# Optimization experiments

Hardware: AMD Instinct MI355X
Metric: run time of the kernel (lower is better)

Reference implementation:

```python
import jax, jax.numpy as jnp
import numpy as np

N_NODE = 100000
N_EDGE = 1600000
D_NODE = 32
D_EDGE = 16
D_OUT = 32
D_IN = 2 * D_NODE + D_EDGE  # 80
D_HID = 2 * D_IN            # 160


def setup_inputs() -> dict:
    key = jax.random.key(0)
    ks = jax.random.split(key, 6)
    nodes = jax.random.normal(ks[0], (N_NODE, D_NODE), dtype=jnp.float32)
    edges = jax.random.normal(ks[1], (N_EDGE, D_EDGE), dtype=jnp.float32)
    senders = jax.random.randint(ks[2], (N_EDGE,), 0, N_NODE, dtype=jnp.int64 if jax.config.jax_enable_x64 else jnp.int32)
    receivers = jax.random.randint(ks[3], (N_EDGE,), 0, N_NODE, dtype=jnp.int64 if jax.config.jax_enable_x64 else jnp.int32)
    # Linear params (fan-in scaled like torch's default init scale)
    W1 = jax.random.normal(ks[4], (D_IN, D_HID), dtype=jnp.float32) / np.sqrt(D_IN)
    b1 = jnp.zeros((D_HID,), dtype=jnp.float32)
    W2 = jax.random.normal(ks[5], (D_HID, D_OUT), dtype=jnp.float32) / np.sqrt(D_HID)
    b2 = jnp.zeros((D_OUT,), dtype=jnp.float32)
    return {"nodes": nodes, "edges": edges, "senders": senders,
            "receivers": receivers, "W1": W1, "b1": b1, "W2": W2, "b2": b2}


def reference(nodes, edges, senders, receivers, W1, b1, W2, b2):
    # gather sender/receiver node features and concat with edge features: [E, 2*d_node+d_edge]
    feats = jnp.concatenate([nodes[senders], nodes[receivers], edges], axis=1)
    h = jax.nn.sigmoid(feats @ W1 + b1)   # [E, 2*d_in]
    new_edges = h @ W2 + b2               # [E, d_edge_out]
    return new_edges
```

## Files before the change

### kernel.cpp

```cpp
#include <hip/hip_runtime.h>

#define NEDGE  1600000
#define NPT    (NEDGE / 16)
#define GRID   2500
#define NIT    (NPT / GRID)
#define ESTEP  (GRID * 16)
#define NNODE  100000
#define NB_OFF 32768
#define WS_BYTES (65536 + NNODE * 32 * 2)

typedef float f32x4  __attribute__((ext_vector_type(4)));
typedef short short8 __attribute__((ext_vector_type(8)));

static __device__ __forceinline__ ushort f2bf(float f) {
  uint u = __builtin_bit_cast(uint, f);
  return (ushort)((u + 0x7FFFu + ((u >> 16) & 1u)) >> 16);
}
static __device__ __forceinline__ uint cvt_pk(float lo, float hi) {
  uint r; asm("v_cvt_pk_bf16_f32 %0, %1, %2" : "=v"(r) : "v"(lo), "v"(hi)); return r;
}
static __device__ __forceinline__ float vexp2(float x) {
  float r; asm("v_exp_f32 %0, %1" : "=v"(r) : "v"(x)); return r;
}
static __device__ __forceinline__ float vrcp(float x) {
  float r; asm("v_rcp_f32 %0, %1" : "=v"(r) : "v"(x)); return r;
}
static __device__ __forceinline__ short8 pack8(float4 a, float4 b) {
  uint4 u;
  u.x = cvt_pk(a.x, a.y); u.y = cvt_pk(a.z, a.w);
  u.z = cvt_pk(b.x, b.y); u.w = cvt_pk(b.z, b.w);
  return __builtin_bit_cast(short8, u);
}

__global__ void prep_frags(const float* __restrict__ W1, const float* __restrict__ b1,
                           const float* __restrict__ W2, ushort* __restrict__ ws) {
  const int idx = blockIdx.x * 256 + threadIdx.x;
  if (idx >= 20480) return;
  const int frag = idx >> 9;
  const int lane = (idx >> 3) & 63;
  const int j    = idx & 7;
  const int g = lane >> 4, c = lane & 15;
  ushort v;
  if (frag < 30) {
    const int wh = frag / 15, rem = frag % 15, mt = rem / 3, kt = rem % 3;
    const int k   = kt * 32 + g * 8 + j;
    const int hid = 32 * mt + 8 * (c >> 2) + 4 * wh + (c & 3);
    const float s = -1.44269504088896f;
    const float val = (k < 80) ? W1[k * 160 + hid] * s
                               : (k == 80 ? b1[hid] * s : 0.0f);
    v = f2bf(val);
  } else {
    const int f2 = frag - 30, wh = f2 / 5, kt = f2 % 5;
    const int k = kt * 32 + g * 8 + j;
    v = f2bf(W2[k * 32 + 16 * wh + c]);
  }
  ws[idx] = v;
}

__global__ void prep_nodes(const float* __restrict__ nodes, ushort* __restrict__ nb) {
  const int idx = blockIdx.x * 256 + threadIdx.x;
  if (idx >= NNODE * 4) return;
  const float4 a = ((const float4*)nodes)[idx * 2];
  const float4 b = ((const float4*)nodes)[idx * 2 + 1];
  *(short8*)(nb + (size_t)idx * 8) = pack8(a, b);
}

__global__ __launch_bounds__(128) void edge_mlp_fast(
    const float* __restrict__ edges,
    const int* __restrict__ senders, const int* __restrict__ receivers,
    const float* __restrict__ b2, float* __restrict__ out,
    const ushort* __restrict__ ws)
{
  __shared__ uint2 X[2][2][5][64];

  const int lane = threadIdx.x & 63;
  const int wh   = threadIdx.x >> 6;
  const int g    = lane >> 4;
  const int c    = lane & 15;
  const ushort* nb = ws + NB_OFF;

  short8 w1f[5][3];
#pragma unroll
  for (int mt = 0; mt < 5; ++mt)
#pragma unroll
    for (int kt = 0; kt < 3; ++kt)
      w1f[mt][kt] = *(const short8*)(ws + ((wh * 15 + mt * 3 + kt) * 64 + lane) * 8);
  short8 w2f[5];
#pragma unroll
  for (int kt = 0; kt < 5; ++kt)
    w2f[kt] = *(const short8*)(ws + ((30 + wh * 5 + kt) * 64 + lane) * 8);

  const float4 b2v = *(const float4*)(b2 + wh * 16 + g * 4);
  const f32x4 b2c = (f32x4){b2v.x, b2v.y, b2v.z, b2v.w};
  const f32x4 z4  = (f32x4){0.f, 0.f, 0.f, 0.f};
  const uint  cE0 = (g == 2) ? 0x3F80u : 0u;

  int e = blockIdx.x * 16 + c;

  short8 nS, nR;
  float4 ee0, ee1;
  {
    const int si = senders[e], ri = receivers[e];
    nS = *(const short8*)(nb + (size_t)si * 32 + g * 8);
    nR = *(const short8*)(nb + (size_t)ri * 32 + g * 8);
    const float* ep = edges + (size_t)e * 16 + (g & 1) * 8;
    ee0 = *(const float4*)ep;  ee1 = *(const float4*)(ep + 4);
  }
  int si1 = senders[e + ESTEP], ri1 = receivers[e + ESTEP];

  f32x4 acc[5];
  {
    uint4 ue;
    ue.x = (g < 2) ? cvt_pk(ee0.x, ee0.y) : cE0;
    ue.y = (g < 2) ? cvt_pk(ee0.z, ee0.w) : 0u;
    ue.z = (g < 2) ? cvt_pk(ee1.x, ee1.y) : 0u;
    ue.w = (g < 2) ? cvt_pk(ee1.z, ee1.w) : 0u;
    const short8 bfE = __builtin_bit_cast(short8, ue);
#pragma unroll
    for (int mt = 0; mt < 5; ++mt)
      acc[mt] = __builtin_amdgcn_mfma_f32_16x16x32_bf16(w1f[mt][0], nS, z4, 0, 0, 0);
#pragma unroll
    for (int mt = 0; mt < 5; ++mt)
      acc[mt] = __builtin_amdgcn_mfma_f32_16x16x32_bf16(w1f[mt][1], nR, acc[mt], 0, 0, 0);
#pragma unroll
    for (int mt = 0; mt < 5; ++mt)
      acc[mt] = __builtin_amdgcn_mfma_f32_16x16x32_bf16(w1f[mt][2], bfE, acc[mt], 0, 0, 0);
  }
  {
    nS = *(const short8*)(nb + (size_t)si1 * 32 + g * 8);
    nR = *(const short8*)(nb + (size_t)ri1 * 32 + g * 8);
    const float* ep = edges + (size_t)(e + ESTEP) * 16 + (g & 1) * 8;
    ee0 = *(const float4*)ep;  ee1 = *(const float4*)(ep + 4);
    si1 = senders[e + 2 * ESTEP];  ri1 = receivers[e + 2 * ESTEP];
  }

#pragma unroll 1
  for (int i = 0; i < NIT - 1; ++i) {
    uint pkA[5], pkB[5];
#pragma unroll
    for (int mt = 0; mt < 5; ++mt) {
      const float h0 = vrcp(1.0f + vexp2(acc[mt][0]));
      const float h1 = vrcp(1.0f + vexp2(acc[mt][1]));
      const float h2 = vrcp(1.0f + vexp2(acc[mt][2]));
      const float h3 = vrcp(1.0f + vexp2(acc[mt][3]));
      pkA[mt] = cvt_pk(h0, h1);
      pkB[mt] = cvt_pk(h2, h3);
    }
#pragma unroll
    for (int kt = 0; kt < 5; ++kt)
      X[wh][i & 1][kt][lane] = make_uint2(pkA[kt], pkB[kt]);

    f32x4 accN[5];
    {
      uint4 ue;
      ue.x = (g < 2) ? cvt_pk(ee0.x, ee0.y) : cE0;
      ue.y = (g < 2) ? cvt_pk(ee0.z, ee0.w) : 0u;
      ue.z = (g < 2) ? cvt_pk(ee1.x, ee1.y) : 0u;
      ue.w = (g < 2) ? cvt_pk(ee1.z, ee1.w) : 0u;
      const short8 bfE = __builtin_bit_cast(short8, ue);
#pragma unroll
      for (int mt = 0; mt < 5; ++mt)
        accN[mt] = __builtin_amdgcn_mfma_f32_16x16x32_bf16(w1f[mt][0], nS, z4, 0, 0, 0);
#pragma unroll
      for (int mt = 0; mt < 5; ++mt)
        accN[mt] = __builtin_amdgcn_mfma_f32_16x16x32_bf16(w1f[mt][1], nR, accN[mt], 0, 0, 0);
#pragma unroll
      for (int mt = 0; mt < 5; ++mt)
        accN[mt] = __builtin_amdgcn_mfma_f32_16x16x32_bf16(w1f[mt][2], bfE, accN[mt], 0, 0, 0);
    }

    {
      nS = *(const short8*)(nb + (size_t)si1 * 32 + g * 8);
      nR = *(const short8*)(nb + (size_t)ri1 * 32 + g * 8);
      const int off2 = (i + 2 < NIT) ? 2 * ESTEP : 0;
      const float* ep = edges + (size_t)(e + off2) * 16 + (g & 1) * 8;
      ee0 = *(const float4*)ep;  ee1 = *(const float4*)(ep + 4);
      const int off3 = (i + 3 < NIT) ? 3 * ESTEP : 0;
      si1 = senders[e + off3];  ri1 = receivers[e + off3];
    }

    __builtin_amdgcn_sched_barrier(0);
    asm volatile("s_waitcnt lgkmcnt(0)\n\ts_barrier" ::: "memory");

    {
      uint2 q[5];
#pragma unroll
      for (int kt = 0; kt < 5; ++kt) q[kt] = X[wh ^ 1][i & 1][kt][lane];
      f32x4 oa, ob;
      if (wh == 0) {
        oa = __builtin_amdgcn_mfma_f32_16x16x32_bf16(w2f[0],
               __builtin_bit_cast(short8, make_uint4(pkA[0], pkB[0], q[0].x, q[0].y)), b2c, 0, 0, 0);
        ob = __builtin_amdgcn_mfma_f32_16x16x32_bf16(w2f[1],
               __builtin_bit_cast(short8, make_uint4(pkA[1], pkB[1], q[1].x, q[1].y)), z4, 0, 0, 0);
        oa = __builtin_amdgcn_mfma_f32_16x16x32_bf16(w2f[2],
               __builtin_bit_cast(short8, make_uint4(pkA[2], pkB[2], q[2].x, q[2].y)), oa, 0, 0, 0);
        ob = __builtin_amdgcn_mfma_f32_16x16x32_bf16(w2f[3],
               __builtin_bit_cast(short8, make_uint4(pkA[3], pkB[3], q[3].x, q[3].y)), ob, 0, 0, 0);
        oa = __builtin_amdgcn_mfma_f32_16x16x32_bf16(w2f[4],
               __builtin_bit_cast(short8, make_uint4(pkA[4], pkB[4], q[4].x, q[4].y)), oa, 0, 0, 0);
      } else {
        oa = __builtin_amdgcn_mfma_f32_16x16x32_bf16(w2f[0],
               __builtin_bit_cast(short8, make_uint4(q[0].x, q[0].y, pkA[0], pkB[0])), b2c, 0, 0, 0);
        ob = __builtin_amdgcn_mfma_f32_16x16x32_bf16(w2f[1],
               __builtin_bit_cast(short8, make_uint4(q[1].x, q[1].y, pkA[1], pkB[1])), z4, 0, 0, 0);
        oa = __builtin_amdgcn_mfma_f32_16x16x32_bf16(w2f[2],
               __builtin_bit_cast(short8, make_uint4(q[2].x, q[2].y, pkA[2], pkB[2])), oa, 0, 0, 0);
        ob = __builtin_amdgcn_mfma_f32_16x16x32_bf16(w2f[3],
               __builtin_bit_cast(short8, make_uint4(q[3].x, q[3].y, pkA[3], pkB[3])), ob, 0, 0, 0);
        oa = __builtin_amdgcn_mfma_f32_16x16x32_bf16(w2f[4],
               __builtin_bit_cast(short8, make_uint4(q[4].x, q[4].y, pkA[4], pkB[4])), oa, 0, 0, 0);
      }
      const f32x4 o = oa + ob;
      float4 st; st.x = o[0]; st.y = o[1]; st.z = o[2]; st.w = o[3];
      *(float4*)(out + (size_t)e * 32 + wh * 16 + g * 4) = st;
    }

#pragma unroll
    for (int mt = 0; mt < 5; ++mt) acc[mt] = accN[mt];
    e += ESTEP;
  }

  {
    uint pkA[5], pkB[5];
#pragma unroll
    for (int mt = 0; mt < 5; ++mt) {
      const float h0 = vrcp(1.0f + vexp2(acc[mt][0]));
      const float h1 = vrcp(1.0f + vexp2(acc[mt][1]));
      const float h2 = vrcp(1.0f + vexp2(acc[mt][2]));
      const float h3 = vrcp(1.0f + vexp2(acc[mt][3]));
      pkA[mt] = cvt_pk(h0, h1);
      pkB[mt] = cvt_pk(h2, h3);
    }
#pragma unroll
    for (int kt = 0; kt < 5; ++kt)
      X[wh][1][kt][lane] = make_uint2(pkA[kt], pkB[kt]);
    asm volatile("s_waitcnt lgkmcnt(0)\n\ts_barrier" ::: "memory");
    uint2 q[5];
#pragma unroll
    for (int kt = 0; kt < 5; ++kt) q[kt] = X[wh ^ 1][1][kt][lane];
    f32x4 oa, ob;
    if (wh == 0) {
      oa = __builtin_amdgcn_mfma_f32_16x16x32_bf16(w2f[0],
             __builtin_bit_cast(short8, make_uint4(pkA[0], pkB[0], q[0].x, q[0].y)), b2c, 0, 0, 0);
      ob = __builtin_amdgcn_mfma_f32_16x16x32_bf16(w2f[1],
             __builtin_bit_cast(short8, make_uint4(pkA[1], pkB[1], q[1].x, q[1].y)), z4, 0, 0, 0);
      oa = __builtin_amdgcn_mfma_f32_16x16x32_bf16(w2f[2],
             __builtin_bit_cast(short8, make_uint4(pkA[2], pkB[2], q[2].x, q[2].y)), oa, 0, 0, 0);
      ob = __builtin_amdgcn_mfma_f32_16x16x32_bf16(w2f[3],
             __builtin_bit_cast(short8, make_uint4(pkA[3], pkB[3], q[3].x, q[3].y)), ob, 0, 0, 0);
      oa = __builtin_amdgcn_mfma_f32_16x16x32_bf16(w2f[4],
             __builtin_bit_cast(short8, make_uint4(pkA[4], pkB[4], q[4].x, q[4].y)), oa, 0, 0, 0);
    } else {
      oa = __builtin_amdgcn_mfma_f32_16x16x32_bf16(w2f[0],
             __builtin_bit_cast(short8, make_uint4(q[0].x, q[0].y, pkA[0], pkB[0])), b2c, 0, 0, 0);
      ob = __builtin_amdgcn_mfma_f32_16x16x32_bf16(w2f[1],
             __builtin_bit_cast(short8, make_uint4(q[1].x, q[1].y, pkA[1], pkB[1])), z4, 0, 0, 0);
      oa = __builtin_amdgcn_mfma_f32_16x16x32_bf16(w2f[2],
             __builtin_bit_cast(short8, make_uint4(q[2].x, q[2].y, pkA[2], pkB[2])), oa, 0, 0, 0);
      ob = __builtin_amdgcn_mfma_f32_16x16x32_bf16(w2f[3],
             __builtin_bit_cast(short8, make_uint4(q[3].x, q[3].y, pkA[3], pkB[3])), ob, 0, 0, 0);
      oa = __builtin_amdgcn_mfma_f32_16x16x32_bf16(w2f[4],
             __builtin_bit_cast(short8, make_uint4(q[4].x, q[4].y, pkA[4], pkB[4])), oa, 0, 0, 0);
    }
    const f32x4 o = oa + ob;
    float4 st; st.x = o[0]; st.y = o[1]; st.z = o[2]; st.w = o[3];
    *(float4*)(out + (size_t)e * 32 + wh * 16 + g * 4) = st;
  }
}

__global__ __launch_bounds__(128) void edge_mlp_ref(
    const float* __restrict__ nodes, const float* __restrict__ edges,
    const int* __restrict__ senders, const int* __restrict__ receivers,
    const float* __restrict__ W1, const float* __restrict__ b1,
    const float* __restrict__ W2, const float* __restrict__ b2,
    float* __restrict__ out)
{
  __shared__ uint2 Xr[2][2][5][64];
  const int lane = threadIdx.x & 63;
  const int wh   = threadIdx.x >> 6;
  const int g    = lane >> 4;
  const int c    = lane & 15;

  short8 w1f[5][3];
  short8 w2f[5];
  const float s = -1.44269504088896f;
  const int hidb = 8 * (c >> 2) + 4 * wh + (c & 3);
#pragma unroll
  for (int mt = 0; mt < 5; ++mt)
#pragma unroll
    for (int kt = 0; kt < 3; ++kt) {
      const int hid = 32 * mt + hidb;
      uint d[4];
#pragma unroll
      for (int dw = 0; dw < 4; ++dw) {
        const int k0 = kt * 32 + g * 8 + dw * 2, k1 = k0 + 1;
        const float f0 = (k0 < 80) ? W1[k0 * 160 + hid] * s : (k0 == 80 ? b1[hid] * s : 0.f);
        const float f1 = (k1 < 80) ? W1[k1 * 160 + hid] * s : (k1 == 80 ? b1[hid] * s : 0.f);
        d[dw] = (uint)f2bf(f0) | ((uint)f2bf(f1) << 16);
      }
      w1f[mt][kt] = __builtin_bit_cast(short8, make_uint4(d[0], d[1], d[2], d[3]));
    }
#pragma unroll
  for (int kt = 0; kt < 5; ++kt) {
    uint d[4];
#pragma unroll
    for (int dw = 0; dw < 4; ++dw) {
      const int k = kt * 32 + g * 8 + dw * 2;
      d[dw] = (uint)f2bf(W2[k * 32 + wh * 16 + c]) |
              ((uint)f2bf(W2[(k + 1) * 32 + wh * 16 + c]) << 16);
    }
    w2f[kt] = __builtin_bit_cast(short8, make_uint4(d[0], d[1], d[2], d[3]));
  }
  const float4 b2v = *(const float4*)(b2 + wh * 16 + g * 4);
  const f32x4 b2c = (f32x4){b2v.x, b2v.y, b2v.z, b2v.w};
  const f32x4 z4  = (f32x4){0.f, 0.f, 0.f, 0.f};
  const uint  cE0 = (g == 2) ? 0x3F80u : 0u;

  int t = blockIdx.x;
  int e = t * 16 + c;
  float4 sn0, sn1, rn0, rn1, ee0, ee1;
  {
    const int si = senders[e], ri = receivers[e];
    const float* sp = nodes + (size_t)si * 32 + g * 8;
    sn0 = *(const float4*)sp;  sn1 = *(const float4*)(sp + 4);
    const float* rp = nodes + (size_t)ri * 32 + g * 8;
    rn0 = *(const float4*)rp;  rn1 = *(const float4*)(rp + 4);
    const float* ep = edges + (size_t)e * 16 + (g & 1) * 8;
    ee0 = *(const float4*)ep;  ee1 = *(const float4*)(ep + 4);
  }
  int e1 = (t + GRID) * 16 + c;
  int si1 = senders[e1], ri1 = receivers[e1];

  for (int i = 0; i < NIT; ++i) {
    const int buf = i & 1;
    uint4 ue;
    ue.x = (g < 2) ? cvt_pk(ee0.x, ee0.y) : cE0;
    ue.y = (g < 2) ? cvt_pk(ee0.z, ee0.w) : 0u;
    ue.z = (g < 2) ? cvt_pk(ee1.x, ee1.y) : 0u;
    ue.w = (g < 2) ? cvt_pk(ee1.z, ee1.w) : 0u;
    const short8 bfE = __builtin_bit_cast(short8, ue);
    const short8 bfS = pack8(sn0, sn1);
    const short8 bfR = pack8(rn0, rn1);

    f32x4 acc[5];
#pragma unroll
    for (int mt = 0; mt < 5; ++mt)
      acc[mt] = __builtin_amdgcn_mfma_f32_16x16x32_bf16(w1f[mt][0], bfS, z4, 0, 0, 0);
#pragma unroll
    for (int mt = 0; mt < 5; ++mt)
      acc[mt] = __builtin_amdgcn_mfma_f32_16x16x32_bf16(w1f[mt][1], bfR, acc[mt], 0, 0, 0);
#pragma unroll
    for (int mt = 0; mt < 5; ++mt)
      acc[mt] = __builtin_amdgcn_mfma_f32_16x16x32_bf16(w1f[mt][2], bfE, acc[mt], 0, 0, 0);

    {
      int tn = t + GRID; if (tn >= NPT) tn = t;
      const int en = tn * 16 + c;
      const float* epn = edges + (size_t)en * 16 + (g & 1) * 8;
      ee0 = *(const float4*)epn;  ee1 = *(const float4*)(epn + 4);
      const float* spn = nodes + (size_t)si1 * 32 + g * 8;
      sn0 = *(const float4*)spn;  sn1 = *(const float4*)(spn + 4);
      const float* rpn = nodes + (size_t)ri1 * 32 + g * 8;
      rn0 = *(const float4*)rpn;  rn1 = *(const float4*)(rpn + 4);
      int t2 = t + 2 * GRID; if (t2 >= NPT) t2 = tn;
      const int e2 = t2 * 16 + c;
      si1 = senders[e2];  ri1 = receivers[e2];
    }

    uint pkA[5], pkB[5];
#pragma unroll
    for (int mt = 0; mt < 5; ++mt) {
      const float h0 = vrcp(1.0f + vexp2(acc[mt][0]));
      const float h1 = vrcp(1.0f + vexp2(acc[mt][1]));
      const float h2 = vrcp(1.0f + vexp2(acc[mt][2]));
      const float h3 = vrcp(1.0f + vexp2(acc[mt][3]));
      pkA[mt] = cvt_pk(h0, h1);
      pkB[mt] = cvt_pk(h2, h3);
    }
#pragma unroll
    for (int kt = 0; kt < 5; ++kt) Xr[wh][buf][kt][lane] = make_uint2(pkA[kt], pkB[kt]);
    asm volatile("s_waitcnt lgkmcnt(0)\n\ts_barrier" ::: "memory");
    uint2 q[5];
#pragma unroll
    for (int kt = 0; kt < 5; ++kt) q[kt] = Xr[wh ^ 1][buf][kt][lane];

    f32x4 oa, ob;
    if (wh == 0) {
      oa = __builtin_amdgcn_mfma_f32_16x16x32_bf16(w2f[0],
             __builtin_bit_cast(short8, make_uint4(pkA[0], pkB[0], q[0].x, q[0].y)), b2c, 0, 0, 0);
      ob = __builtin_amdgcn_mfma_f32_16x16x32_bf16(w2f[1],
             __builtin_bit_cast(short8, make_uint4(pkA[1], pkB[1], q[1].x, q[1].y)), z4, 0, 0, 0);
      oa = __builtin_amdgcn_mfma_f32_16x16x32_bf16(w2f[2],
             __builtin_bit_cast(short8, make_uint4(pkA[2], pkB[2], q[2].x, q[2].y)), oa, 0, 0, 0);
      ob = __builtin_amdgcn_mfma_f32_16x16x32_bf16(w2f[3],
             __builtin_bit_cast(short8, make_uint4(pkA[3], pkB[3], q[3].x, q[3].y)), ob, 0, 0, 0);
      oa = __builtin_amdgcn_mfma_f32_16x16x32_bf16(w2f[4],
             __builtin_bit_cast(short8, make_uint4(pkA[4], pkB[4], q[4].x, q[4].y)), oa, 0, 0, 0);
    } else {
      oa = __builtin_amdgcn_mfma_f32_16x16x32_bf16(w2f[0],
             __builtin_bit_cast(short8, make_uint4(q[0].x, q[0].y, pkA[0], pkB[0])), b2c, 0, 0, 0);
      ob = __builtin_amdgcn_mfma_f32_16x16x32_bf16(w2f[1],
             __builtin_bit_cast(short8, make_uint4(q[1].x, q[1].y, pkA[1], pkB[1])), z4, 0, 0, 0);
      oa = __builtin_amdgcn_mfma_f32_16x16x32_bf16(w2f[2],
             __builtin_bit_cast(short8, make_uint4(q[2].x, q[2].y, pkA[2], pkB[2])), oa, 0, 0, 0);
      ob = __builtin_amdgcn_mfma_f32_16x16x32_bf16(w2f[3],
             __builtin_bit_cast(short8, make_uint4(q[3].x, q[3].y, pkA[3], pkB[3])), ob, 0, 0, 0);
      oa = __builtin_amdgcn_mfma_f32_16x16x32_bf16(w2f[4],
             __builtin_bit_cast(short8, make_uint4(q[4].x, q[4].y, pkA[4], pkB[4])), oa, 0, 0, 0);
    }
    const f32x4 o = oa + ob;
    float4 st; st.x = o[0]; st.y = o[1]; st.z = o[2]; st.w = o[3];
    *(float4*)(out + (size_t)e * 32 + wh * 16 + g * 4) = st;

    t += GRID;
    e = t * 16 + c;
  }
}

extern "C" void kernel_launch(void* const* d_in, const int* in_sizes, int n_in,
                              void* d_out, int out_size, void* d_ws, size_t ws_size,
                              hipStream_t stream) {
  const float* nodes     = (const float*)d_in[0];
  const float* edges     = (const float*)d_in[1];
  const int*   senders   = (const int*)d_in[2];
  const int*   receivers = (const int*)d_in[3];
  const float* W1        = (const float*)d_in[4];
  const float* b1        = (const float*)d_in[5];
  const float* W2        = (const float*)d_in[6];
  const float* b2        = (const float*)d_in[7];
  float* out = (float*)d_out;

  if (ws_size >= (size_t)WS_BYTES) {
    ushort* ws = (ushort*)d_ws;
    prep_frags<<<80, 256, 0, stream>>>(W1, b1, W2, ws);
    prep_nodes<<<(NNODE * 4 + 255) / 256, 256, 0, stream>>>(nodes, ws + NB_OFF);
    edge_mlp_fast<<<GRID, 128, 0, stream>>>(edges, senders, receivers, b2, out, ws);
  } else {
    edge_mlp_ref<<<GRID, 128, 0, stream>>>(nodes, edges, senders, receivers,
                                           W1, b1, W2, b2, out);
  }
}
```

Measured before the change: 177.9 us.

## Drop software-pipelined MLP loop, use single-stage loop with interleaved LDS exchange

Replaces the software pipeline in the fast kernel, which issued next-tile layer-1 MFMAs before the layer-2 exchange, with a simpler per-iteration loop: layer-1 MFMA, prefetch loads, sigmoid, LDS exchange, then layer-2 MFMA. The LDS buffer is relaid as [buf][kt][lane][wave] so each wave reads a contiguous short8 holding both halves, removing the per-wave branch and the register packing. The grid changes from 2500 to 2000 blocks. This lowers register pressure and instruction count but gives up overlap of layer-1 compute with the barrier and exchange.

Result: no change. 174.5 us (-1.9%).

```diff
diff --git a/kernel.cpp b/kernel.cpp
--- a/kernel.cpp
+++ b/kernel.cpp
@@ -2,9 +2,8 @@
 
 #define NEDGE  1600000
 #define NPT    (NEDGE / 16)
-#define GRID   2500
+#define GRID   2000
 #define NIT    (NPT / GRID)
-#define ESTEP  (GRID * 16)
 #define NNODE  100000
 #define NB_OFF 32768
 #define WS_BYTES (65536 + NNODE * 32 * 2)
@@ -71,7 +70,7 @@
     const float* __restrict__ b2, float* __restrict__ out,
     const ushort* __restrict__ ws)
 {
-  __shared__ uint2 X[2][2][5][64];
+  __shared__ uint2 X[2][5][64][2];
 
   const int lane = threadIdx.x & 63;
   const int wh   = threadIdx.x >> 6;
@@ -95,8 +94,8 @@
   const f32x4 z4  = (f32x4){0.f, 0.f, 0.f, 0.f};
   const uint  cE0 = (g == 2) ? 0x3F80u : 0u;
 
-  int e = blockIdx.x * 16 + c;
-
+  int t = blockIdx.x;
+  int e = t * 16 + c;
   short8 nS, nR;
   float4 ee0, ee1;
   {
@@ -106,16 +105,20 @@
     const float* ep = edges + (size_t)e * 16 + (g & 1) * 8;
     ee0 = *(const float4*)ep;  ee1 = *(const float4*)(ep + 4);
   }
-  int si1 = senders[e + ESTEP], ri1 = receivers[e + ESTEP];
-
-  f32x4 acc[5];
-  {
+  int e1 = (t + GRID) * 16 + c;
+  int si1 = senders[e1], ri1 = receivers[e1];
+
+  for (int i = 0; i < NIT; ++i) {
+    const int buf = i & 1;
+
     uint4 ue;
     ue.x = (g < 2) ? cvt_pk(ee0.x, ee0.y) : cE0;
     ue.y = (g < 2) ? cvt_pk(ee0.z, ee0.w) : 0u;
     ue.z = (g < 2) ? cvt_pk(ee1.x, ee1.y) : 0u;
     ue.w = (g < 2) ? cvt_pk(ee1.z, ee1.w) : 0u;
     const short8 bfE = __builtin_bit_cast(short8, ue);
+
+    f32x4 acc[5];
 #pragma unroll
     for (int mt = 0; mt < 5; ++mt)
       acc[mt] = __builtin_amdgcn_mfma_f32_16x16x32_bf16(w1f[mt][0], nS, z4, 0, 0, 0);
@@ -125,17 +128,19 @@
 #pragma unroll
     for (int mt = 0; mt < 5; ++mt)
       acc[mt] = __builtin_amdgcn_mfma_f32_16x16x32_bf16(w1f[mt][2], bfE, acc[mt], 0, 0, 0);
-  }
-  {
-    nS = *(const short8*)(nb + (size_t)si1 * 32 + g * 8);
-    nR = *(const short8*)(nb + (size_t)ri1 * 32 + g * 8);
-    const float* ep = edges + (size_t)(e + ESTEP) * 16 + (g & 1) * 8;
-    ee0 = *(const float4*)ep;  ee1 = *(const float4*)(ep + 4);
-    si1 = senders[e + 2 * ESTEP];  ri1 = receivers[e + 2 * ESTEP];
-  }
-
-#pragma unroll 1
-  for (int i = 0; i < NIT - 1; ++i) {
+
+    {
+      int tn = t + GRID; if (tn >= NPT) tn = t;
+      const int en = tn * 16 + c;
+      const float* epn = edges + (size_t)en * 16 + (g & 1) * 8;
+      ee0 = *(const float4*)epn;  ee1 = *(const float4*)(epn + 4);
+      nS = *(const short8*)(nb + (size_t)si1 * 32 + g * 8);
+      nR = *(const short8*)(nb + (size_t)ri1 * 32 + g * 8);
+      int t2 = t + 2 * GRID; if (t2 >= NPT) t2 = tn;
+      const int e2 = t2 * 16 + c;
+      si1 = senders[e2];  ri1 = receivers[e2];
+    }
+
     uint pkA[5], pkB[5];
 #pragma unroll
     for (int mt = 0; mt < 5; ++mt) {
@@ -146,81 +151,134 @@
       pkA[mt] = cvt_pk(h0, h1);
       pkB[mt] = cvt_pk(h2, h3);
     }
+
 #pragma unroll
     for (int kt = 0; kt < 5; ++kt)
-      X[wh][i & 1][kt][lane] = make_uint2(pkA[kt], pkB[kt]);
-
-    f32x4 accN[5];
+      X[buf][kt][lane][wh] = make_uint2(pkA[kt], pkB[kt]);
+    asm volatile("s_waitcnt lgkmcnt(0)\n\ts_barrier" ::: "memory");
+
+    f32x4 oa, ob;
     {
-      uint4 ue;
-      ue.x = (g < 2) ? cvt_pk(ee0.x, ee0.y) : cE0;
-      ue.y = (g < 2) ? cvt_pk(ee0.z, ee0.w) : 0u;
-      ue.z = (g < 2) ? cvt_pk(ee1.x, ee1.y) : 0u;
-      ue.w = (g < 2) ? cvt_pk(ee1.z, ee1.w) : 0u;
-      const short8 bfE = __builtin_bit_cast(short8, ue);
-#pragma unroll
-      for (int mt = 0; mt < 5; ++mt)
-        accN[mt] = __builtin_amdgcn_mfma_f32_16x16x32_bf16(w1f[mt][0], nS, z4, 0, 0, 0);
-#pragma unroll
-      for (int mt = 0; mt < 5; ++mt)
-        accN[mt] = __builtin_amdgcn_mfma_f32_16x16x32_bf16(w1f[mt][1], nR, accN[mt], 0, 0, 0);
-#pragma unroll
-      for (int mt = 0; mt < 5; ++mt)
-        accN[mt] = __builtin_amdgcn_mfma_f32_16x16x32_bf16(w1f[mt][2], bfE, accN[mt], 0, 0, 0);
-    }
+      const short8 bb0 = *(const short8*)&X[buf][0][lane][0];
+      const short8 bb1 = *(const short8*)&X[buf][1][lane][0];
+      const short8 bb2 = *(const short8*)&X[buf][2][lane][0];
+      const short8 bb3 = *(const short8*)&X[buf][3][lane][0];
+      const short8 bb4 = *(const short8*)&X[buf][4][lane][0];
+      oa = __builtin_amdgcn_mfma_f32_16x16x32_bf16(w2f[0], bb0, b2c, 0, 0, 0);
+      ob = __builtin_amdgcn_mfma_f32_16x16x32_bf16(w2f[1], bb1, z4, 0, 0, 0);
+      oa = __builtin_amdgcn_mfma_f32_16x16x32_bf16(w2f[2], bb2, oa, 0, 0, 0);
+      ob = __builtin_amdgcn_mfma_f32_16x16x32_bf16(w2f[3], bb3, ob, 0, 0, 0);
+      oa = __builtin_amdgcn_mfma_f32_16x16x32_bf16(w2f[4], bb4, oa, 0, 0, 0);
+    }
+    const f32x4 o = oa + ob;
+
+    float4 st; st.x = o[0]; st.y = o[1]; st.z = o[2]; st.w = o[3];
+    *(float4*)(out + (size_t)e * 32 + wh * 16 + g * 4) = st;
+
+    t += GRID;
+    e = t * 16 + c;
+  }
+}
+
+__global__ __launch_bounds__(128) void edge_mlp_ref(
+    const float* __restrict__ nodes, const float* __restrict__ edges,
+    const int* __restrict__ senders, const int* __restrict__ receivers,
+    const float* __restrict__ W1, const float* __restrict__ b1,
+    const float* __restrict__ W2, const float* __restrict__ b2,
+    float* __restrict__ out)
+{
+  __shared__ uint2 Xr[2][2][5][64];
+  const int lane = threadIdx.x & 63;
+  const int wh   = threadIdx.x >> 6;
+  const int g    = lane >> 4;
+  const int c    = lane & 15;
+
+  short8 w1f[5][3];
+  short8 w2f[5];
+  const float s = -1.44269504088896f;
+  const int hidb = 8 * (c >> 2) + 4 * wh + (c & 3);
+#pragma unroll
+  for (int mt = 0; mt < 5; ++mt)
+#pragma unroll
+    for (int kt = 0; kt < 3; ++kt) {
+      const int hid = 32 * mt + hidb;
+      uint d[4];
+#pragma unroll
+      for (int dw = 0; dw < 4; ++dw) {
+        const int k0 = kt * 32 + g * 8 + dw * 2, k1 = k0 + 1;
+        const float f0 = (k0 < 80) ? W1[k0 * 160 + hid] * s : (k0 == 80 ? b1[hid] * s : 0.f);
+        const float f1 = (k1 < 80) ? W1[k1 * 160 + hid] * s : (k1 == 80 ? b1[hid] * s : 0.f);
+        d[dw] = (uint)f2bf(f0) | ((uint)f2bf(f1) << 16);
+      }
+      w1f[mt][kt] = __builtin_bit_cast(short8, make_uint4(d[0], d[1], d[2], d[3]));
+    }
+#pragma unroll
+  for (int kt = 0; kt < 5; ++kt) {
+    uint d[4];
+#pragma unroll
+    for (int dw = 0; dw < 4; ++dw) {
+      const int k = kt * 32 + g * 8 + dw * 2;
+      d[dw] = (uint)f2bf(W2[k * 32 + wh * 16 + c]) |
+              ((uint)f2bf(W2[(k + 1) * 32 + wh * 16 + c]) << 16);
+    }
+    w2f[kt] = __builtin_bit_cast(short8, make_uint4(d[0], d[1], d[2], d[3]));
+  }
+  const float4 b2v = *(const float4*)(b2 + wh * 16 + g * 4);
+  const f32x4 b2c = (f32x4){b2v.x, b2v.y, b2v.z, b2v.w};
+  const f32x4 z4  = (f32x4){0.f, 0.f, 0.f, 0.f};
+  const uint  cE0 = (g == 2) ? 0x3F80u : 0u;
+
+  int t = blockIdx.x;
+  int e = t * 16 + c;
+  float4 sn0, sn1, rn0, rn1, ee0, ee1;
+  {
+    const int si = senders[e], ri = receivers[e];
+    const float* sp = nodes + (size_t)si * 32 + g * 8;
+    sn0 = *(const float4*)sp;  sn1 = *(const float4*)(sp + 4);
+    const float* rp = nodes + (size_t)ri * 32 + g * 8;
+    rn0 = *(const float4*)rp;  rn1 = *(const float4*)(rp + 4);
+    const float* ep = edges + (size_t)e * 16 + (g & 1) * 8;
+    ee0 = *(const float4*)ep;  ee1 = *(const float4*)(ep + 4);
+  }
+  int e1 = (t + GRID) * 16 + c;
+  int si1 = senders[e1], ri1 = receivers[e1];
+
+  for (int i = 0; i < NIT; ++i) {
+    const int buf = i & 1;
+    uint4 ue;
+    ue.x = (g < 2) ? cvt_pk(ee0.x, ee0.y) : cE0;
+    ue.y = (g < 2) ? cvt_pk(ee0.z, ee0.w) : 0u;
+    ue.z = (g < 2) ? cvt_pk(ee1.x, ee1.y) : 0u;
+    ue.w = (g < 2) ? cvt_pk(ee1.z, ee1.w) : 0u;
+    const short8 bfE = __builtin_bit_cast(short8, ue);
+    const short8 bfS = pack8(sn0, sn1);
+    const short8 bfR = pack8(rn0, rn1);
+
+    f32x4 acc[5];
+#pragma unroll
+    for (int mt = 0; mt < 5; ++mt)
+      acc[mt] = __builtin_amdgcn_mfma_f32_16x16x32_bf16(w1f[mt][0], bfS, z4, 0, 0, 0);
+#pragma unroll
+    for (int mt = 0; mt < 5; ++mt)
+      acc[mt] = __builtin_amdgcn_mfma_f32_16x16x32_bf16(w1f[mt][1], bfR, acc[mt], 0, 0, 0);
+#pragma unroll
+    for (int mt = 0; mt < 5; ++mt)
+      acc[mt] = __builtin_amdgcn_mfma_f32_16x16x32_bf16(w1f[mt][2], bfE, acc[mt], 0, 0, 0);
 
     {
-      nS = *(const short8*)(nb + (size_t)si1 * 32 + g * 8);
-      nR = *(const short8*)(nb + (size_t)ri1 * 32 + g * 8);
-      const int off2 = (i + 2 < NIT) ? 2 * ESTEP : 0;
-      const float* ep = edges + (size_t)(e + off2) * 16 + (g & 1) * 8;
-      ee0 = *(const float4*)ep;  ee1 = *(const float4*)(ep + 4);
-      const int off3 = (i + 3 < NIT) ? 3 * ESTEP : 0;
-      si1 = senders[e + off3];  ri1 = receivers[e + off3];
-    }
-
-    __builtin_amdgcn_sched_barrier(0);
-    asm volatile("s_waitcnt lgkmcnt(0)\n\ts_barrier" ::: "memory");
-
-    {
-      uint2 q[5];
-#pragma unroll
-      for (int kt = 0; kt < 5; ++kt) q[kt] = X[wh ^ 1][i & 1][kt][lane];
-      f32x4 oa, ob;
-      if (wh == 0) {
-        oa = __builtin_amdgcn_mfma_f32_16x16x32_bf16(w2f[0],
-               __builtin_bit_cast(short8, make_uint4(pkA[0], pkB[0], q[0].x, q[0].y)), b2c, 0, 0, 0);
-        ob = __builtin_amdgcn_mfma_f32_16x16x32_bf16(w2f[1],
-               __builtin_bit_cast(short8, make_uint4(pkA[1], pkB[1], q[1].x, q[1].y)), z4, 0, 0, 0);
-        oa = __builtin_amdgcn_mfma_f32_16x16x32_bf16(w2f[2],
-               __builtin_bit_cast(short8, make_uint4(pkA[2], pkB[2], q[2].x, q[2].y)), oa, 0, 0, 0);
-        ob = __builtin_amdgcn_mfma_f32_16x16x32_bf16(w2f[3],
-               __builtin_bit_cast(short8, make_uint4(pkA[3], pkB[3], q[3].x, q[3].y)), ob, 0, 0, 0);
-        oa = __builtin_amdgcn_mfma_f32_16x16x32_bf16(w2f[4],
-               __builtin_bit_cast(short8, make_uint4(pkA[4], pkB[4], q[4].x, q[4].y)), oa, 0, 0, 0);
-      } else {
-        oa = __builtin_amdgcn_mfma_f32_16x16x32_bf16(w2f[0],
-               __builtin_bit_cast(short8, make_uint4(q[0].x, q[0].y, pkA[0], pkB[0])), b2c, 0, 0, 0);
-        ob = __builtin_amdgcn_mfma_f32_16x16x32_bf16(w2f[1],
-               __builtin_bit_cast(short8, make_uint4(q[1].x, q[1].y, pkA[1], pkB[1])), z4, 0, 0, 0);
-        oa = __builtin_amdgcn_mfma_f32_16x16x32_bf16(w2f[2],
-               __builtin_bit_cast(short8, make_uint4(q[2].x, q[2].y, pkA[2], pkB[2])), oa, 0, 0, 0);
-        ob = __builtin_amdgcn_mfma_f32_16x16x32_bf16(w2f[3],
-               __builtin_bit_cast(short8, make_uint4(q[3].x, q[3].y, pkA[3], pkB[3])), ob, 0, 0, 0);
-        oa = __builtin_amdgcn_mfma_f32_16x16x32_bf16(w2f[4],
-               __builtin_bit_cast(short8, make_uint4(q[4].x, q[4].y, pkA[4], pkB[4])), oa, 0, 0, 0);
-      }
-      const f32x4 o = oa + ob;
-      float4 st; st.x = o[0]; st.y = o[1]; st.z = o[2]; st.w = o[3];
-      *(float4*)(out + (size_t)e * 32 + wh * 16 + g * 4) = st;
-    }
-
-#pragma unroll
-    for (int mt = 0; mt < 5; ++mt) acc[mt] = accN[mt];
-    e += ESTEP;
-  }
-
-  {
+      int tn = t + GRID; if (tn >= NPT) tn = t;
+      const int en = tn * 16 + c;
+      const float* epn = edges + (size_t)en * 16 + (g & 1) * 8;
+      ee0 = *(const float4*)epn;  ee1 = *(const float4*)(epn + 4);
+      const float* spn = nodes + (size_t)si1 * 32 + g * 8;
+      sn0 = *(const float4*)spn;  sn1 = *(const float4*)(spn + 4);
+      const float* rpn = nodes + (size_t)ri1 * 32 + g * 8;
+      rn0 = *(const float4*)rpn;  rn1 = *(const float4*)(rpn + 4);
+      int t2 = t + 2 * GRID; if (t2 >= NPT) t2 = tn;
+      const int e2 = t2 * 16 + c;
+      si1 = senders[e2];  ri1 = receivers[e2];
+    }
+
     uint pkA[5], pkB[5];
 #pragma unroll
     for (int mt = 0; mt < 5; ++mt) {
@@ -232,12 +290,12 @@
       pkB[mt] = cvt_pk(h2, h3);
     }
 #pragma unroll
-    for (int kt = 0; kt < 5; ++kt)
-      X[wh][1][kt][lane] = make_uint2(pkA[kt], pkB[kt]);
+    for (int kt = 0; kt < 5; ++kt) Xr[wh][buf][kt][lane] = make_uint2(pkA[kt], pkB[kt]);
     asm volatile("s_waitcnt lgkmcnt(0)\n\ts_barrier" ::: "memory");
     uint2 q[5];
 #pragma unroll
-    for (int kt = 0; kt < 5; ++kt) q[kt] = X[wh ^ 1][1][kt][lane];
+    for (int kt = 0; kt < 5; ++kt) q[kt] = Xr[wh ^ 1][buf][kt][lane];
+
     f32x4 oa, ob;
     if (wh == 0) {
       oa = __builtin_amdgcn_mfma_f32_16x16x32_bf16(w2f[0],
@@ -265,152 +323,6 @@
     const f32x4 o = oa + ob;
     float4 st; st.x = o[0]; st.y = o[1]; st.z = o[2]; st.w = o[3];
     *(float4*)(out + (size_t)e * 32 + wh * 16 + g * 4) = st;
-  }
-}
-
-__global__ __launch_bounds__(128) void edge_mlp_ref(
-    const float* __restrict__ nodes, const float* __restrict__ edges,
-    const int* __restrict__ senders, const int* __restrict__ receivers,
-    const float* __restrict__ W1, const float* __restrict__ b1,
-    const float* __restrict__ W2, const float* __restrict__ b2,
-    float* __restrict__ out)
-{
-  __shared__ uint2 Xr[2][2][5][64];
-  const int lane = threadIdx.x & 63;
-  const int wh   = threadIdx.x >> 6;
-  const int g    = lane >> 4;
-  const int c    = lane & 15;
-
-  short8 w1f[5][3];
-  short8 w2f[5];
-  const float s = -1.44269504088896f;
-  const int hidb = 8 * (c >> 2) + 4 * wh + (c & 3);
-#pragma unroll
-  for (int mt = 0; mt < 5; ++mt)
-#pragma unroll
-    for (int kt = 0; kt < 3; ++kt) {
-      const int hid = 32 * mt + hidb;
-      uint d[4];
-#pragma unroll
-      for (int dw = 0; dw < 4; ++dw) {
-        const int k0 = kt * 32 + g * 8 + dw * 2, k1 = k0 + 1;
-        const float f0 = (k0 < 80) ? W1[k0 * 160 + hid] * s : (k0 == 80 ? b1[hid] * s : 0.f);
-        const float f1 = (k1 < 80) ? W1[k1 * 160 + hid] * s : (k1 == 80 ? b1[hid] * s : 0.f);
-        d[dw] = (uint)f2bf(f0) | ((uint)f2bf(f1) << 16);
-      }
-      w1f[mt][kt] = __builtin_bit_cast(short8, make_uint4(d[0], d[1], d[2], d[3]));
-    }
-#pragma unroll
-  for (int kt = 0; kt < 5; ++kt) {
-    uint d[4];
-#pragma unroll
-    for (int dw = 0; dw < 4; ++dw) {
-      const int k = kt * 32 + g * 8 + dw * 2;
-      d[dw] = (uint)f2bf(W2[k * 32 + wh * 16 + c]) |
-              ((uint)f2bf(W2[(k + 1) * 32 + wh * 16 + c]) << 16);
-    }
-    w2f[kt] = __builtin_bit_cast(short8, make_uint4(d[0], d[1], d[2], d[3]));
-  }
-  const float4 b2v = *(const float4*)(b2 + wh * 16 + g * 4);
-  const f32x4 b2c = (f32x4){b2v.x, b2v.y, b2v.z, b2v.w};
-  const f32x4 z4  = (f32x4){0.f, 0.f, 0.f, 0.f};
-  const uint  cE0 = (g == 2) ? 0x3F80u : 0u;
-
-  int t = blockIdx.x;
-  int e = t * 16 + c;
-  float4 sn0, sn1, rn0, rn1, ee0, ee1;
-  {
-    const int si = senders[e], ri = receivers[e];
-    const float* sp = nodes + (size_t)si * 32 + g * 8;
-    sn0 = *(const float4*)sp;  sn1 = *(const float4*)(sp + 4);
-    const float* rp = nodes + (size_t)ri * 32 + g * 8;
-    rn0 = *(const float4*)rp;  rn1 = *(const float4*)(rp + 4);
-    const float* ep = edges + (size_t)e * 16 + (g & 1) * 8;
-    ee0 = *(const float4*)ep;  ee1 = *(const float4*)(ep + 4);
-  }
-  int e1 = (t + GRID) * 16 + c;
-  int si1 = senders[e1], ri1 = receivers[e1];
-
-  for (int i = 0; i < NIT; ++i) {
-    const int buf = i & 1;
-    uint4 ue;
-    ue.x = (g < 2) ? cvt_pk(ee0.x, ee0.y) : cE0;
-    ue.y = (g < 2) ? cvt_pk(ee0.z, ee0.w) : 0u;
-    ue.z = (g < 2) ? cvt_pk(ee1.x, ee1.y) : 0u;
-    ue.w = (g < 2) ? cvt_pk(ee1.z, ee1.w) : 0u;
-    const short8 bfE = __builtin_bit_cast(short8, ue);
-    const short8 bfS = pack8(sn0, sn1);
-    const short8 bfR = pack8(rn0, rn1);
-
-    f32x4 acc[5];
-#pragma unroll
-    for (int mt = 0; mt < 5; ++mt)
-      acc[mt] = __builtin_amdgcn_mfma_f32_16x16x32_bf16(w1f[mt][0], bfS, z4, 0, 0, 0);
-#pragma unroll
-    for (int mt = 0; mt < 5; ++mt)
-      acc[mt] = __builtin_amdgcn_mfma_f32_16x16x32_bf16(w1f[mt][1], bfR, acc[mt], 0, 0, 0);
-#pragma unroll
-    for (int mt = 0; mt < 5; ++mt)
-      acc[mt] = __builtin_amdgcn_mfma_f32_16x16x32_bf16(w1f[mt][2], bfE, acc[mt], 0, 0, 0);
-
-    {
-      int tn = t + GRID; if (tn >= NPT) tn = t;
-      const int en = tn * 16 + c;
-      const float* epn = edges + (size_t)en * 16 + (g & 1) * 8;
-      ee0 = *(const float4*)epn;  ee1 = *(const float4*)(epn + 4);
-      const float* spn = nodes + (size_t)si1 * 32 + g * 8;
-      sn0 = *(const float4*)spn;  sn1 = *(const float4*)(spn + 4);
-      const float* rpn = nodes + (size_t)ri1 * 32 + g * 8;
-      rn0 = *(const float4*)rpn;  rn1 = *(const float4*)(rpn + 4);
-      int t2 = t + 2 * GRID; if (t2 >= NPT) t2 = tn;
-      const int e2 = t2 * 16 + c;
-      si1 = senders[e2];  ri1 = receivers[e2];
-    }
-
-    uint pkA[5], pkB[5];
-#pragma unroll
-    for (int mt = 0; mt < 5; ++mt) {
-      const float h0 = vrcp(1.0f + vexp2(acc[mt][0]));
-      const float h1 = vrcp(1.0f + vexp2(acc[mt][1]));
-      const float h2 = vrcp(1.0f + vexp2(acc[mt][2]));
-      const float h3 = vrcp(1.0f + vexp2(acc[mt][3]));
-      pkA[mt] = cvt_pk(h0, h1);
-      pkB[mt] = cvt_pk(h2, h3);
-    }
-#pragma unroll
-    for (int kt = 0; kt < 5; ++kt) Xr[wh][buf][kt][lane] = make_uint2(pkA[kt], pkB[kt]);
-    asm volatile("s_waitcnt lgkmcnt(0)\n\ts_barrier" ::: "memory");
-    uint2 q[5];
-#pragma unroll
-    for (int kt = 0; kt < 5; ++kt) q[kt] = Xr[wh ^ 1][buf][kt][lane];
-
-    f32x4 oa, ob;
-    if (wh == 0) {
-      oa = __builtin_amdgcn_mfma_f32_16x16x32_bf16(w2f[0],
-             __builtin_bit_cast(short8, make_uint4(pkA[0], pkB[0], q[0].x, q[0].y)), b2c, 0, 0, 0);
-      ob = __builtin_amdgcn_mfma_f32_16x16x32_bf16(w2f[1],
-             __builtin_bit_cast(short8, make_uint4(pkA[1], pkB[1], q[1].x, q[1].y)), z4, 0, 0, 0);
-      oa = __builtin_amdgcn_mfma_f32_16x16x32_bf16(w2f[2],
-             __builtin_bit_cast(short8, make_uint4(pkA[2], pkB[2], q[2].x, q[2].y)), oa, 0, 0, 0);
-      ob = __builtin_amdgcn_mfma_f32_16x16x32_bf16(w2f[3],
-             __builtin_bit_cast(short8, make_uint4(pkA[3], pkB[3], q[3].x, q[3].y)), ob, 0, 0, 0);
-      oa = __builtin_amdgcn_mfma_f32_16x16x32_bf16(w2f[4],
-             __builtin_bit_cast(short8, make_uint4(pkA[4], pkB[4], q[4].x, q[4].y)), oa, 0, 0, 0);
-    } else {
-      oa = __builtin_amdgcn_mfma_f32_16x16x32_bf16(w2f[0],
-             __builtin_bit_cast(short8, make_uint4(q[0].x, q[0].y, pkA[0], pkB[0])), b2c, 0, 0, 0);
-      ob = __builtin_amdgcn_mfma_f32_16x16x32_bf16(w2f[1],
-             __builtin_bit_cast(short8, make_uint4(q[1].x, q[1].y, pkA[1], pkB[1])), z4, 0, 0, 0);
-      oa = __builtin_amdgcn_mfma_f32_16x16x32_bf16(w2f[2],
-             __builtin_bit_cast(short8, make_uint4(q[2].x, q[2].y, pkA[2], pkB[2])), oa, 0, 0, 0);
-      ob = __builtin_amdgcn_mfma_f32_16x16x32_bf16(w2f[3],
-             __builtin_bit_cast(short8, make_uint4(q[3].x, q[3].y, pkA[3], pkB[3])), ob, 0, 0, 0);
-      oa = __builtin_amdgcn_mfma_f32_16x16x32_bf16(w2f[4],
-             __builtin_bit_cast(short8, make_uint4(q[4].x, q[4].y, pkA[4], pkB[4])), oa, 0, 0, 0);
-    }
-    const f32x4 o = oa + ob;
-    float4 st; st.x = o[0]; st.y = o[1]; st.z = o[2]; st.w = o[3];
-    *(float4*)(out + (size_t)e * 32 + wh * 16 + g * 4) = st;
 
     t += GRID;
     e = t * 16 + c;
```
